# Kernel optimization log

Hardware: AMD Instinct MI355X
Metric: run time of the kernel (lower is better)

## Reference

```python
import jax, jax.numpy as jnp
import numpy as np

B, S, H, R = 32, 512, 1024, 64


def _bernoulli(key, shape, p=0.05):
    return (jax.random.uniform(key, shape) < p).astype(jnp.float32)


def setup_inputs() -> dict:
    key = jax.random.key(0)
    ks = jax.random.split(key, 16)
    context = jax.random.normal(ks[0], (B, S, H), dtype=jnp.float32)
    masks = jnp.ones((B, S), dtype=jnp.float32)
    all_subject_heads = _bernoulli(ks[1], (B, S))
    all_subject_tails = _bernoulli(ks[2], (B, S))
    # one-hot subject head/tail positions (tail >= head)
    h_pos = jax.random.randint(ks[3], (B,), 0, S // 2)
    t_pos = h_pos + jax.random.randint(ks[4], (B,), 0, 8)
    subject_head = jax.nn.one_hot(h_pos, S, dtype=jnp.float32)
    subject_tail = jax.nn.one_hot(t_pos, S, dtype=jnp.float32)
    object_heads = _bernoulli(ks[5], (B, S, R))
    object_tails = _bernoulli(ks[6], (B, S, R))
    # learned parameters (PyTorch Linear: y = x @ W.T + b; store as [in, out])
    sc = 1.0 / np.sqrt(H)
    Ws_h = jax.random.uniform(ks[7], (H, 1), minval=-sc, maxval=sc)
    bs_h = jnp.zeros((1,), dtype=jnp.float32)
    Ws_t = jax.random.uniform(ks[8], (H, 1), minval=-sc, maxval=sc)
    bs_t = jnp.zeros((1,), dtype=jnp.float32)
    Wo_h = jax.random.uniform(ks[9], (H, R), minval=-sc, maxval=sc)
    bo_h = jnp.zeros((R,), dtype=jnp.float32)
    Wo_t = jax.random.uniform(ks[10], (H, R), minval=-sc, maxval=sc)
    bo_t = jnp.zeros((R,), dtype=jnp.float32)
    return dict(context=context, masks=masks,
                all_subject_heads=all_subject_heads, all_subject_tails=all_subject_tails,
                subject_head=subject_head, subject_tail=subject_tail,
                object_heads=object_heads, object_tails=object_tails,
                Ws_h=Ws_h, bs_h=bs_h, Ws_t=Ws_t, bs_t=bs_t,
                Wo_h=Wo_h, bo_h=bo_h, Wo_t=Wo_t, bo_t=bo_t)


def _bce_with_logits(logits, targets):
    # numerically stable, matches F.binary_cross_entropy_with_logits(reduction='none')
    return jnp.maximum(logits, 0.0) - logits * targets + jnp.log1p(jnp.exp(-jnp.abs(logits)))


def _masked_loss(gold, pred, mask):
    loss = _bce_with_logits(pred, gold)
    if loss.ndim != mask.ndim:
        mask = mask[..., None]
    return jnp.sum(loss * mask) / jnp.sum(mask)


def reference(context, masks, all_subject_heads, all_subject_tails,
              subject_head, subject_tail, object_heads, object_tails,
              Ws_h, bs_h, Ws_t, bs_t, Wo_h, bo_h, Wo_t, bo_t):
    # subject logits: [B,S]
    pred_subject_heads = (context @ Ws_h + bs_h)[..., 0]
    pred_subject_tails = (context @ Ws_t + bs_t)[..., 0]
    # subject pooling: one-hot [B,S] x context [B,S,H] -> [B,H]
    sub_h = jnp.einsum('bs,bsh->bh', subject_head, context)
    sub_t = jnp.einsum('bs,bsh->bh', subject_tail, context)
    subject = (sub_h + sub_t) * 0.5
    context_subject = context + subject[:, None, :]  # [B,S,H]
    pred_object_heads = context_subject @ Wo_h + bo_h  # [B,S,R]
    pred_object_tails = context_subject @ Wo_t + bo_t  # [B,S,R]
    loss = (_masked_loss(all_subject_heads, pred_subject_heads, masks)
            + _masked_loss(all_subject_tails, pred_subject_tails, masks)
            + _masked_loss(object_heads, pred_object_heads, masks)
            + _masked_loss(object_tails, pred_object_tails, masks))
    return loss
```

## Files before the change

### kernel.cpp

```cpp
#include <hip/hip_runtime.h>


#define B_  32
#define S_  512
#define H_  1024
#define R_  64
#define M_  (B_ * S_)
#define NPAD 160
#define NVALID 130
#define BK 64
#define BKP 72
#define MT 32
#define NCHUNK (H_ / BK)
#define TBLK 20

typedef __attribute__((ext_vector_type(4))) float  floatx4;
typedef __attribute__((ext_vector_type(8))) short  short8;
typedef __attribute__((ext_vector_type(4))) unsigned short u16x4;
typedef __attribute__((ext_vector_type(8))) unsigned short u16x8;

__device__ __forceinline__ unsigned short f2bf(float f) {
    unsigned int u = __float_as_uint(f);
    u = (u + 0x7FFFu + ((u >> 16) & 1u)) >> 16;
    return (unsigned short)u;
}

__device__ __forceinline__ void gload_lds16(const unsigned short* g, unsigned short* l) {
    __builtin_amdgcn_global_load_lds(
        (const __attribute__((address_space(1))) unsigned int*)g,
        (__attribute__((address_space(3))) unsigned int*)l, 16, 0, 0);
}

__global__ __launch_bounds__(256) void aux_kernel(
        const float* __restrict__ ctx, const float* __restrict__ head,
        const float* __restrict__ tail, const float* __restrict__ masks,
        const float* __restrict__ Wo_h, const float* __restrict__ Wo_t,
        const float* __restrict__ Ws_h, const float* __restrict__ Ws_t,
        const float* __restrict__ bo_h, const float* __restrict__ bo_t,
        const float* __restrict__ bs_h, const float* __restrict__ bs_t,
        unsigned short* __restrict__ WtG, float* __restrict__ rowBias,
        float* __restrict__ accum) {
    const int tid = threadIdx.x;
    __shared__ float tr[32][257];
    __shared__ float subj[H_];
    __shared__ float partS[4][256];
    __shared__ int cnt;
    __shared__ int   sidx[8];
    __shared__ float sw[8];

    if (blockIdx.x < TBLK) {
        const int kt = blockIdx.x / 5, nt = blockIdx.x % 5;
        const int k0 = kt * 256, n0 = nt * 32;
        if (n0 < 128) {
            const float* src = (n0 < 64) ? Wo_h : Wo_t;
            const int cb = n0 & 63;
            const int nn = tid & 31, kk = tid >> 5;
#pragma unroll
            for (int i = 0; i < 32; ++i) {
                const int k = k0 + i * 8 + kk;
                tr[nn][i * 8 + kk] = src[(size_t)k * R_ + cb + nn];
            }
            __syncthreads();
#pragma unroll
            for (int p = 0; p < 4; ++p) {
                const int chunk = p * 256 + tid;
                const int n = chunk >> 5;
                const int kc = (chunk & 31) * 8;
                u16x8 v;
#pragma unroll
                for (int j = 0; j < 8; ++j) v[j] = f2bf(tr[n][kc + j]);
                *(u16x8*)(WtG + (size_t)(n0 + n) * H_ + k0 + kc) = v;
            }
        } else {
#pragma unroll
            for (int p = 0; p < 4; ++p) {
                const int chunk = p * 256 + tid;
                const int n = 128 + (chunk >> 5);
                const int kc = (chunk & 31) * 8;
                u16x8 v;
#pragma unroll
                for (int j = 0; j < 8; ++j) {
                    float f = (n == 128) ? Ws_h[k0 + kc + j]
                            : (n == 129) ? Ws_t[k0 + kc + j] : 0.0f;
                    v[j] = f2bf(f);
                }
                *(u16x8*)(WtG + (size_t)n * H_ + k0 + kc) = v;
            }
        }
        return;
    }

    const int b = blockIdx.x - TBLK;
    if (tid == 0) cnt = 0;
    __syncthreads();
    float msk = 0.0f;
    for (int s = tid; s < S_; s += 256) {
        float w = 0.5f * (head[b * S_ + s] + tail[b * S_ + s]);
        if (w != 0.0f) {
            int i = atomicAdd(&cnt, 1);
            if (i < 8) { sidx[i] = s; sw[i] = w; }
        }
        msk += masks[b * S_ + s];
    }
    for (int o = 32; o > 0; o >>= 1) msk += __shfl_down(msk, o, 64);
    if ((tid & 63) == 0) atomicAdd(&accum[1], msk);
    __syncthreads();
    const int nnz = cnt < 8 ? cnt : 8;
    for (int h = tid; h < H_; h += 256) {
        float a = 0.0f;
        for (int i = 0; i < nnz; i++)
            a += sw[i] * ctx[((size_t)b * S_ + sidx[i]) * H_ + h];
        subj[h] = a;
    }
    __syncthreads();
    {
        const int cg = tid & 31;
        const int ks = tid >> 5;
        const int c4 = cg * 4;
        const float* W = (c4 < 64) ? Wo_h : Wo_t;
        const int cc = c4 & 63;
        const int kk0 = ks * 128;
        float ax = 0.f, ay = 0.f, az = 0.f, aw = 0.f;
#pragma unroll 4
        for (int k = kk0; k < kk0 + 128; ++k) {
            const float4 w = *(const float4*)(W + (size_t)k * R_ + cc);
            const float sv = subj[k];
            ax += sv * w.x; ay += sv * w.y; az += sv * w.z; aw += sv * w.w;
        }
        partS[0][tid] = ax; partS[1][tid] = ay;
        partS[2][tid] = az; partS[3][tid] = aw;
    }
    __syncthreads();
    if (tid < NPAD) {
        float bias = tid < 64  ? bo_h[tid]
                   : tid < 128 ? bo_t[tid - 64]
                   : tid == 128 ? bs_h[0]
                   : tid == 129 ? bs_t[0] : 0.0f;
        float a2 = 0.0f;
        if (tid < 128) {
            const int g = tid >> 2, j = tid & 3;
#pragma unroll
            for (int s = 0; s < 8; ++s) a2 += partS[j][s * 32 + g];
        }
        rowBias[b * NPAD + tid] = bias + a2;
    }
}

__global__ __launch_bounds__(256, 2) void main_kernel(
        const float* __restrict__ ctx, const unsigned short* __restrict__ WtG,
        const float* __restrict__ rowBias, const float* __restrict__ masks,
        const float* __restrict__ ash, const float* __restrict__ ast,
        const float* __restrict__ oh, const float* __restrict__ ot,
        float* __restrict__ accum, float* __restrict__ out) {
    __shared__ __align__(16) unsigned short Asm[2][MT * BKP];
    __shared__ __align__(16) unsigned short Bsm[2][NPAD * BK];
    __shared__ float rbuf[4];

    const int tid  = threadIdx.x;
    const int gm0  = blockIdx.x * MT;
    const int b    = gm0 >> 9;
    const int wave = tid >> 6, lane = tid & 63;
    const int wm = wave & 1;
    const int wn = wave >> 1;
    const int lr = lane & 15, q = lane >> 4;

    const int ar = tid >> 4, af = tid & 15;
    const float* aSrc = ctx + (size_t)(gm0 + ar) * H_ + af * 4;
    unsigned short* aD0 = &Asm[0][ar * BKP + af * 4];
    unsigned short* aD1 = &Asm[1][ar * BKP + af * 4];

    const int br = tid >> 3, bc = (tid & 7) * 16;
    const int bswz = bc ^ ((br & 7) << 4);
    const unsigned short* bSrc = WtG + (size_t)br * H_ + (bswz >> 1);
    const int bDstOff = br * 64 + (bc >> 1);

    const int aOff = (wm * 16 + lr) * BKP + q * 8;
    int bOff[5];
#pragma unroll
    for (int tt = 0; tt < 5; ++tt) {
        const int row = wn * 80 + tt * 16 + lr;
        bOff[tt] = row * 128 + ((q * 16) ^ ((row & 7) << 4));
    }

    floatx4 acc[5];
#pragma unroll
    for (int tt = 0; tt < 5; ++tt) acc[tt] = (floatx4){0.f, 0.f, 0.f, 0.f};

    {
        float4 v0 = *(const float4*)(aSrc);
        float4 v1 = *(const float4*)(aSrc + 16 * H_);
#pragma unroll
        for (int p = 0; p < 5; ++p)
            gload_lds16(bSrc + (size_t)p * 32 * H_, &Bsm[0][p * 2048 + bDstOff]);
        u16x4 u0 = { f2bf(v0.x), f2bf(v0.y), f2bf(v0.z), f2bf(v0.w) };
        u16x4 u1 = { f2bf(v1.x), f2bf(v1.y), f2bf(v1.z), f2bf(v1.w) };
        *(u16x4*)aD0 = u0;
        *(u16x4*)(aD0 + 16 * BKP) = u1;
    }
    __syncthreads();

    int cur = 0;
    for (int t = 0; t < NCHUNK; ++t) {
        const int nk = (t + 1) * BK;
        float4 v0, v1;
        if (t < NCHUNK - 1) {
            v0 = *(const float4*)(aSrc + nk);
            v1 = *(const float4*)(aSrc + 16 * H_ + nk);
            unsigned short* bN = &Bsm[cur ^ 1][0];
#pragma unroll
            for (int p = 0; p < 5; ++p)
                gload_lds16(bSrc + (size_t)p * 32 * H_ + nk, bN + p * 2048 + bDstOff);
        }
        const unsigned short* Ac = &Asm[cur][0];
        const char* Bc = (const char*)&Bsm[cur][0];
#pragma unroll
        for (int kk = 0; kk < BK; kk += 32) {
            short8 afr = *(const short8*)&Ac[aOff + kk];
#pragma unroll
            for (int tt = 0; tt < 5; ++tt) {
                short8 bfr = *(const short8*)(Bc + (bOff[tt] ^ (kk << 1)));
                acc[tt] = __builtin_amdgcn_mfma_f32_16x16x32_bf16(afr, bfr, acc[tt], 0, 0, 0);
            }
        }
        if (t < NCHUNK - 1) {
            unsigned short* aDN = cur ? aD0 : aD1;
            u16x4 u0 = { f2bf(v0.x), f2bf(v0.y), f2bf(v0.z), f2bf(v0.w) };
            u16x4 u1 = { f2bf(v1.x), f2bf(v1.y), f2bf(v1.z), f2bf(v1.w) };
            *(u16x4*)aDN = u0;
            *(u16x4*)(aDN + 16 * BKP) = u1;
            __syncthreads();
            cur ^= 1;
        }
    }

    float lsum = 0.0f;
#pragma unroll
    for (int tt = 0; tt < 5; ++tt) {
        const int col = wn * 80 + tt * 16 + lr;
        if (col < NVALID) {
            const float rb = rowBias[b * NPAD + col];
#pragma unroll
            for (int i = 0; i < 4; ++i) {
                const int row = gm0 + wm * 16 + q * 4 + i;
                const float l = acc[tt][i] + rb;
                float tgt;
                if (col < 64)        tgt = oh[(size_t)row * R_ + col];
                else if (col < 128)  tgt = ot[(size_t)row * R_ + (col - 64)];
                else if (col == 128) tgt = ash[row];
                else                 tgt = ast[row];
                const float mk = masks[row];
                const float bce = fmaxf(l, 0.0f) - l * tgt + log1pf(__expf(-fabsf(l)));
                lsum += bce * mk;
            }
        }
    }
    for (int o = 32; o > 0; o >>= 1) lsum += __shfl_down(lsum, o, 64);
    if (lane == 0) rbuf[wave] = lsum;
    __syncthreads();
    if (tid == 0) {
        atomicAdd(&accum[0], rbuf[0] + rbuf[1] + rbuf[2] + rbuf[3]);
        __threadfence();
        const unsigned int prev = atomicAdd((unsigned int*)(accum + 2), 1u);
        if (prev == gridDim.x - 1) {
            const float s = atomicAdd(&accum[0], 0.0f);
            const float m = atomicAdd(&accum[1], 0.0f);
            out[0] = s / m;
        }
    }
}

extern "C" void kernel_launch(void* const* d_in, const int* in_sizes, int n_in,
                              void* d_out, int out_size, void* d_ws, size_t ws_size,
                              hipStream_t stream) {
    const float* ctx   = (const float*)d_in[0];
    const float* masks = (const float*)d_in[1];
    const float* ash   = (const float*)d_in[2];
    const float* ast   = (const float*)d_in[3];
    const float* sh    = (const float*)d_in[4];
    const float* st    = (const float*)d_in[5];
    const float* oh    = (const float*)d_in[6];
    const float* ot    = (const float*)d_in[7];
    const float* Ws_h  = (const float*)d_in[8];
    const float* bs_h  = (const float*)d_in[9];
    const float* Ws_t  = (const float*)d_in[10];
    const float* bs_t  = (const float*)d_in[11];
    const float* Wo_h  = (const float*)d_in[12];
    const float* bo_h  = (const float*)d_in[13];
    const float* Wo_t  = (const float*)d_in[14];
    const float* bo_t  = (const float*)d_in[15];
    float* out = (float*)d_out;

    char* ws = (char*)d_ws;
    float* accum   = (float*)(ws + 0);
    float* rowBias = (float*)(ws + 256);
    unsigned short* WtG = (unsigned short*)(ws + 256 + 32 * NPAD * 4);

    hipMemsetAsync(accum, 0, 12, stream);
    aux_kernel<<<TBLK + B_, 256, 0, stream>>>(ctx, sh, st, masks, Wo_h, Wo_t,
                                              Ws_h, Ws_t, bo_h, bo_t, bs_h, bs_t,
                                              WtG, rowBias, accum);
    main_kernel<<<M_ / MT, 256, 0, stream>>>(ctx, WtG, rowBias, masks,
                                             ash, ast, oh, ot, accum, out);
}
```

Baseline: 167.9 us.

## Stage GEMM tiles through registers with single LDS buffer and larger K chunk

Replaces the double-buffered LDS pipeline (direct global-to-LDS loads for B, register staging for A) with a register-prefetch scheme. Each iteration writes the previously loaded A and B chunk into a single LDS buffer, issues global loads for the next chunk into registers, and then runs the MFMAs. The K chunk doubles to 128, which halves the loop trip count and barrier count. In exchange there are two barriers per iteration, higher register pressure from holding 4 float4 plus 10 u16x8 values, and B no longer uses the async global_load_lds path.

```diff
diff --git a/kernel.cpp b/kernel.cpp
--- a/kernel.cpp
+++ b/kernel.cpp
@@ -8,8 +8,8 @@
 #define M_  (B_ * S_)
 #define NPAD 160
 #define NVALID 130
-#define BK 64
-#define BKP 72
+#define BK 128
+#define BKP 136
 #define MT 32
 #define NCHUNK (H_ / BK)
 #define TBLK 20
@@ -25,10 +25,11 @@
     return (unsigned short)u;
 }
 
-__device__ __forceinline__ void gload_lds16(const unsigned short* g, unsigned short* l) {
-    __builtin_amdgcn_global_load_lds(
-        (const __attribute__((address_space(1))) unsigned int*)g,
-        (__attribute__((address_space(3))) unsigned int*)l, 16, 0, 0);
+__device__ __forceinline__ u16x8 cvt8u(float4 a, float4 b) {
+    u16x8 u;
+    u[0] = f2bf(a.x); u[1] = f2bf(a.y); u[2] = f2bf(a.z); u[3] = f2bf(a.w);
+    u[4] = f2bf(b.x); u[5] = f2bf(b.y); u[6] = f2bf(b.z); u[7] = f2bf(b.w);
+    return u;
 }
 
 __global__ __launch_bounds__(256) void aux_kernel(
@@ -120,15 +121,15 @@
         const float* W = (c4 < 64) ? Wo_h : Wo_t;
         const int cc = c4 & 63;
         const int kk0 = ks * 128;
-        float ax = 0.f, ay = 0.f, az = 0.f, aw = 0.f;
+        float ax = 0.f, ay = 0.f, az = 0.f, aw2 = 0.f;
 #pragma unroll 4
         for (int k = kk0; k < kk0 + 128; ++k) {
             const float4 w = *(const float4*)(W + (size_t)k * R_ + cc);
             const float sv = subj[k];
-            ax += sv * w.x; ay += sv * w.y; az += sv * w.z; aw += sv * w.w;
+            ax += sv * w.x; ay += sv * w.y; az += sv * w.z; aw2 += sv * w.w;
         }
         partS[0][tid] = ax; partS[1][tid] = ay;
-        partS[2][tid] = az; partS[3][tid] = aw;
+        partS[2][tid] = az; partS[3][tid] = aw2;
     }
     __syncthreads();
     if (tid < NPAD) {
@@ -152,8 +153,8 @@
         const float* __restrict__ ash, const float* __restrict__ ast,
         const float* __restrict__ oh, const float* __restrict__ ot,
         float* __restrict__ accum, float* __restrict__ out) {
-    __shared__ __align__(16) unsigned short Asm[2][MT * BKP];
-    __shared__ __align__(16) unsigned short Bsm[2][NPAD * BK];
+    __shared__ __align__(16) unsigned short Asm[MT * BKP];
+    __shared__ __align__(16) unsigned short Bsm[NPAD * BK];
     __shared__ float rbuf[4];
 
     const int tid  = threadIdx.x;
@@ -164,74 +165,69 @@
     const int wn = wave >> 1;
     const int lr = lane & 15, q = lane >> 4;
 
-    const int ar = tid >> 4, af = tid & 15;
-    const float* aSrc = ctx + (size_t)(gm0 + ar) * H_ + af * 4;
-    unsigned short* aD0 = &Asm[0][ar * BKP + af * 4];
-    unsigned short* aD1 = &Asm[1][ar * BKP + af * 4];
-
-    const int br = tid >> 3, bc = (tid & 7) * 16;
-    const int bswz = bc ^ ((br & 7) << 4);
-    const unsigned short* bSrc = WtG + (size_t)br * H_ + (bswz >> 1);
-    const int bDstOff = br * 64 + (bc >> 1);
+    const int ar = tid >> 3, as_ = (tid & 7) * 16;
+    const float* aSrc = ctx + (size_t)(gm0 + ar) * H_ + as_;
+    unsigned short* aDst = &Asm[ar * BKP + as_];
+
+    const int br = tid >> 3, bs0 = (tid & 7) * 16;
+    const unsigned short* bSrc = WtG + (size_t)br * H_ + bs0;
+    const int bswz = (br & 7) << 4;
+    char* bDstB = (char*)Bsm + br * 256;
 
     const int aOff = (wm * 16 + lr) * BKP + q * 8;
     int bOff[5];
 #pragma unroll
     for (int tt = 0; tt < 5; ++tt) {
         const int row = wn * 80 + tt * 16 + lr;
-        bOff[tt] = row * 128 + ((q * 16) ^ ((row & 7) << 4));
+        bOff[tt] = row * 256 + ((q * 16) ^ ((row & 7) << 4));
     }
 
     floatx4 acc[5];
 #pragma unroll
     for (int tt = 0; tt < 5; ++tt) acc[tt] = (floatx4){0.f, 0.f, 0.f, 0.f};
 
-    {
-        float4 v0 = *(const float4*)(aSrc);
-        float4 v1 = *(const float4*)(aSrc + 16 * H_);
-#pragma unroll
-        for (int p = 0; p < 5; ++p)
-            gload_lds16(bSrc + (size_t)p * 32 * H_, &Bsm[0][p * 2048 + bDstOff]);
-        u16x4 u0 = { f2bf(v0.x), f2bf(v0.y), f2bf(v0.z), f2bf(v0.w) };
-        u16x4 u1 = { f2bf(v1.x), f2bf(v1.y), f2bf(v1.z), f2bf(v1.w) };
-        *(u16x4*)aD0 = u0;
-        *(u16x4*)(aD0 + 16 * BKP) = u1;
-    }
-    __syncthreads();
-
-    int cur = 0;
+    float4 aR[4];
+    u16x8  bR[10];
+
+#define LOADREGS(k0) do {                                                      \
+        _Pragma("unroll")                                                      \
+        for (int i = 0; i < 4; ++i)                                            \
+            aR[i] = *(const float4*)(aSrc + (k0) + i * 4);                     \
+        _Pragma("unroll")                                                      \
+        for (int p = 0; p < 5; ++p) {                                          \
+            bR[2*p]   = *(const u16x8*)(bSrc + (size_t)(p*32) * H_ + (k0));    \
+            bR[2*p+1] = *(const u16x8*)(bSrc + (size_t)(p*32) * H_ + (k0) + 8);\
+        }                                                                      \
+    } while (0)
+
+#define WRITE_LDS() do {                                                       \
+        *(u16x8*)(aDst)     = cvt8u(aR[0], aR[1]);                             \
+        *(u16x8*)(aDst + 8) = cvt8u(aR[2], aR[3]);                             \
+        _Pragma("unroll")                                                      \
+        for (int p = 0; p < 5; ++p) {                                          \
+            *(u16x8*)(bDstB + p * 32 * 256 + ((bs0 * 2)      ^ bswz)) = bR[2*p];   \
+            *(u16x8*)(bDstB + p * 32 * 256 + ((bs0 * 2 + 16) ^ bswz)) = bR[2*p+1]; \
+        }                                                                      \
+    } while (0)
+
+    LOADREGS(0);
     for (int t = 0; t < NCHUNK; ++t) {
-        const int nk = (t + 1) * BK;
-        float4 v0, v1;
-        if (t < NCHUNK - 1) {
-            v0 = *(const float4*)(aSrc + nk);
-            v1 = *(const float4*)(aSrc + 16 * H_ + nk);
-            unsigned short* bN = &Bsm[cur ^ 1][0];
-#pragma unroll
-            for (int p = 0; p < 5; ++p)
-                gload_lds16(bSrc + (size_t)p * 32 * H_ + nk, bN + p * 2048 + bDstOff);
-        }
-        const unsigned short* Ac = &Asm[cur][0];
-        const char* Bc = (const char*)&Bsm[cur][0];
+        __syncthreads();
+        WRITE_LDS();
+        if (t < NCHUNK - 1) LOADREGS((t + 1) * BK);
+        __syncthreads();
 #pragma unroll
         for (int kk = 0; kk < BK; kk += 32) {
-            short8 afr = *(const short8*)&Ac[aOff + kk];
+            short8 afr = *(const short8*)&Asm[aOff + kk];
 #pragma unroll
             for (int tt = 0; tt < 5; ++tt) {
-                short8 bfr = *(const short8*)(Bc + (bOff[tt] ^ (kk << 1)));
+                short8 bfr = *(const short8*)((const char*)Bsm + (bOff[tt] ^ (kk << 1)));
                 acc[tt] = __builtin_amdgcn_mfma_f32_16x16x32_bf16(afr, bfr, acc[tt], 0, 0, 0);
             }
         }
-        if (t < NCHUNK - 1) {
-            unsigned short* aDN = cur ? aD0 : aD1;
-            u16x4 u0 = { f2bf(v0.x), f2bf(v0.y), f2bf(v0.z), f2bf(v0.w) };
-            u16x4 u1 = { f2bf(v1.x), f2bf(v1.y), f2bf(v1.z), f2bf(v1.w) };
-            *(u16x4*)aDN = u0;
-            *(u16x4*)(aDN + 16 * BKP) = u1;
-            __syncthreads();
-            cur ^= 1;
-        }
-    }
+    }
+#undef LOADREGS
+#undef WRITE_LDS
 
     float lsum = 0.0f;
 #pragma unroll
```

Measured after the change: 165.4 us. Within noise of the previous version (-1.5%).
